# Optimization experiments

Measured on AMD Instinct MI355X. Metric: run time of the kernel, lower is better.

The kernel has to match this reference:

```python
import jax, jax.numpy as jnp
import numpy as np
import math

MU = 5; ETA = 1.0; ITERS = 3
SIGMA_C = 1.0; SIGMA_S = 1.6 * SIGMA_C
SIGMA_M = 3.0; RHO = 0.99; TAU = 0.7
MAX_T = int(math.floor(3 * SIGMA_C))  # 3
MAX_S = int(math.floor(3 * SIGMA_M))  # 9
DELTA = 1.0
B, C, X, Y = 4, 1, 512, 512


def _gpdf(v, sig):
    return math.exp(-v * v / (2.0 * sig * sig)) / (math.sqrt(2.0 * math.pi) * sig)


def _sobel(img):
    k = jnp.array([[-1., -2., -1.], [0., 0., 0.], [1., 2., 1.]], dtype=img.dtype)
    kern = jnp.stack([k, k.T])[:, None]  # [2,1,3,3] OIHW
    return jax.lax.conv_general_dilated(img, kern, (1, 1), [(1, 1), (1, 1)],
                                        dimension_numbers=('NCHW', 'OIHW', 'NCHW'))


def _gather_flat(arr, idx):
    # arr [b,c,x,y], idx int [b,x,y] flattened spatial index (px*Y+py)
    b, c, x, y = arr.shape
    flat = arr.reshape(b, c, x * y)
    idxb = jnp.broadcast_to(idx.reshape(b, 1, x * y), (b, c, x * y))
    return jnp.take_along_axis(flat, idxb, axis=2).reshape(b, c, x, y)


def _safe_norm(v):
    m = jnp.linalg.norm(v, axis=1, keepdims=True)
    return v / jnp.where(m == 0, 1.0, m)


def _etf(images):
    b, c, x, y = images.shape
    sob = _sobel(images)                                   # [b,2,x,y]
    mag = jnp.linalg.norm(sob, axis=1, keepdims=True)      # [b,1,x,y]
    mag = mag / jnp.max(mag)
    mag_p = jnp.pad(mag, ((0, 0), (0, 0), (MU, MU), (MU, MU)))
    sobel_X = mag[:, None]                                 # [b,1,1,x,y]
    tang = _safe_norm(jnp.stack([-sob[:, 1], sob[:, 0]], axis=1))
    K = 2 * MU + 1
    for _ in range(ITERS):
        for ori in ('V', 'H'):
            tang_p = jnp.pad(tang, ((0, 0), (0, 0), (MU, MU), (MU, MU)))
            tang_X = tang[:, None]                         # [b,1,2,x,y]
            if ori == 'V':
                tang_Y = jnp.stack([tang_p[:, :, i:i + x, MU:MU + y] for i in range(K)], axis=1)
                sobel_Y = jnp.stack([mag_p[:, :, i:i + x, MU:MU + y] for i in range(K)], axis=1)
            else:
                tang_Y = jnp.stack([tang_p[:, :, MU:MU + x, i:i + y] for i in range(K)], axis=1)
                sobel_Y = jnp.stack([mag_p[:, :, MU:MU + x, i:i + y] for i in range(K)], axis=1)
            # weight: magnitude term * direction term / 2
            w = (jnp.tanh(ETA * (sobel_Y - sobel_X)) + 1.0) \
                * jnp.sum(tang_X * tang_Y, axis=2, keepdims=True) * 0.5
            tang = _safe_norm(jnp.sum(tang_Y * w, axis=1))
    return tang


def _dog(images, etf):
    b, c, x, y = images.shape
    xi, yi = jnp.meshgrid(jnp.arange(x, dtype=images.dtype),
                          jnp.arange(y, dtype=images.dtype), indexing='ij')
    idx0 = jnp.broadcast_to(jnp.stack([xi, yi])[None], (b, 2, x, y))
    per = jnp.stack([-etf[:, 1], etf[:, 0]], axis=1)       # perpendicular to flow
    dog = jnp.zeros_like(images)
    tw = 0.0
    for t in range(-MAX_T, MAX_T + 1):
        pts = idx0 + DELTA * per * t
        px = jnp.round(jnp.clip(pts[:, 0], 0, x - 1)).astype(jnp.int32)
        py = jnp.round(jnp.clip(pts[:, 1], 0, y - 1)).astype(jnp.int32)
        il = _gather_flat(images, px * y + py)
        gw = _gpdf(t, SIGMA_C) - RHO * _gpdf(t, SIGMA_S)
        tw += gw
        dog = dog + il * gw
    return dog / tw


def _fdog_float(images):
    b, c, x, y = images.shape
    etf = _etf(images)
    dog = _dog(images, etf)
    fdog = jnp.zeros_like(images)
    tw = 0.0
    xi, yi = jnp.meshgrid(jnp.arange(x, dtype=jnp.int32),
                          jnp.arange(y, dtype=jnp.int32), indexing='ij')
    for s_dir in (-1, 1):
        px = jnp.broadcast_to(xi[None], (b, x, y))
        py = jnp.broadcast_to(yi[None], (b, x, y))
        for s in range(0 if s_dir == 1 else 1, MAX_S + 1):
            if s != 0:
                p_etf = _gather_flat(etf, px * y + py)     # flow at current points
                fx = px.astype(images.dtype) + DELTA * p_etf[:, 0] * s_dir
                fy = py.astype(images.dtype) + DELTA * p_etf[:, 1] * s_dir
                px = jnp.round(jnp.clip(fx, 0, x - 1)).astype(jnp.int32)
                py = jnp.round(jnp.clip(fy, 0, y - 1)).astype(jnp.int32)
            f_s = _gather_flat(dog, px * y + py)
            gw = _gpdf(s, SIGMA_M)
            tw += gw
            fdog = fdog + f_s * gw
    return fdog / tw


def setup_inputs() -> dict:
    key = jax.random.key(0)
    images = jax.random.uniform(key, (B, C, X, Y), dtype=jnp.float32)
    return {"images": images}


def reference(images):
    fdog = _fdog_float(images)
    edges = ~((fdog < 0) & (1.0 + jnp.tanh(fdog) < TAU))
    return edges.astype(jnp.int32)
```

## Files before the change

kernel.cpp:

```cpp
#include <hip/hip_runtime.h>
#include <math.h>

#pragma clang fp contract(off)

#define BN 4
#define SX 512
#define SY 512
#define NPIX (BN * SX * SY)
#define MU 5
#define MB (1024 * 1024)
#define NBLOCKS 2048

struct DogW  { float g[7];  float tw; };
struct FdogW { float g[10]; float tw; };

__device__ __forceinline__ float fast_tanh_f32(float dF) {
    double d = (double)dF;
    double y = fabs(d);
    double t = expm1(2.0 * y);
    double r = t / (t + 2.0);
    if (y > 350.0) r = 1.0;
    return (float)copysign(r, d);
}

__device__ __forceinline__ float img_at(const float* __restrict__ img, int b, int x, int y) {
    if (x < 0 || x >= SX || y < 0 || y >= SY) return 0.0f;
    return img[(size_t)b * SX * SY + (size_t)x * SY + y];
}

#define SLAB_DECODE                                   \
    int slab = blockIdx.x;                            \
    int b    = slab >> 1;                             \
    int xi   = ((slab & 1) << 8) + blockIdx.y;        \
    size_t base = (size_t)b * SX * SY;                \
    size_t rowb = base + (size_t)xi * SY;

__global__ __launch_bounds__(256) void k_sobel(const float* __restrict__ img,
                                               float* __restrict__ mag,
                                               float2* __restrict__ tang,
                                               float* __restrict__ partial) {
#pragma clang fp contract(off)
    SLAB_DECODE
    float bmax = 0.0f;
#pragma unroll
    for (int half = 0; half < 2; ++half) {
        int yi = (int)threadIdx.x + half * 256;

        float v00 = img_at(img, b, xi - 1, yi - 1);
        float v01 = img_at(img, b, xi - 1, yi    );
        float v02 = img_at(img, b, xi - 1, yi + 1);
        float v10 = img_at(img, b, xi,     yi - 1);
        float v12 = img_at(img, b, xi,     yi + 1);
        float v20 = img_at(img, b, xi + 1, yi - 1);
        float v21 = img_at(img, b, xi + 1, yi    );
        float v22 = img_at(img, b, xi + 1, yi + 1);

        float s0 = (-1.0f * v00);
        s0 = s0 + (-2.0f * v01);
        s0 = s0 + (-1.0f * v02);
        s0 = s0 + ( 1.0f * v20);
        s0 = s0 + ( 2.0f * v21);
        s0 = s0 + ( 1.0f * v22);
        float s1 = (-1.0f * v00);
        s1 = s1 + ( 1.0f * v02);
        s1 = s1 + (-2.0f * v10);
        s1 = s1 + ( 2.0f * v12);
        s1 = s1 + (-1.0f * v20);
        s1 = s1 + ( 1.0f * v22);

        float m = sqrtf((s0 * s0) + (s1 * s1));
        mag[rowb + yi] = m;

        float tx = -s1, ty = s0;
        float n = sqrtf((tx * tx) + (ty * ty));
        float d = (n == 0.0f) ? 1.0f : n;
        tang[rowb + yi] = make_float2(tx / d, ty / d);
        bmax = fmaxf(bmax, m);
    }

    for (int off = 32; off > 0; off >>= 1) bmax = fmaxf(bmax, __shfl_down(bmax, off, 64));
    __shared__ float red[4];
    int lane = threadIdx.x & 63;
    int wid  = threadIdx.x >> 6;
    if (lane == 0) red[wid] = bmax;
    __syncthreads();
    if (threadIdx.x == 0) {
        float bm = fmaxf(fmaxf(red[0], red[1]), fmaxf(red[2], red[3]));
        partial[blockIdx.x + 8 * blockIdx.y] = bm;
    }
}

__global__ void k_reduce(const float* __restrict__ partial, unsigned int* __restrict__ maxbits) {
    float m = 0.0f;
    for (int i = threadIdx.x; i < NBLOCKS; i += 256) m = fmaxf(m, partial[i]);
    for (int off = 32; off > 0; off >>= 1) m = fmaxf(m, __shfl_down(m, off, 64));
    __shared__ float red[4];
    int lane = threadIdx.x & 63;
    int wid  = threadIdx.x >> 6;
    if (lane == 0) red[wid] = m;
    __syncthreads();
    if (threadIdx.x == 0) {
        float bm = fmaxf(fmaxf(red[0], red[1]), fmaxf(red[2], red[3]));
        *maxbits = __float_as_uint(bm);
    }
}

__global__ void k_norm(float* __restrict__ mag, const unsigned int* __restrict__ maxbits) {
    int i = blockIdx.x * blockDim.x + threadIdx.x;
    float mx = __uint_as_float(*maxbits);
    mag[i] = mag[i] / mx;
}

__global__ __launch_bounds__(256) void k_tanh(const float* __restrict__ mag,
                                              const unsigned int* __restrict__ maxbits,
                                              float* __restrict__ TV, float* __restrict__ TH) {
#pragma clang fp contract(off)
    SLAB_DECODE
    float mx = __uint_as_float(*maxbits);
#pragma unroll
    for (int half = 0; half < 2; ++half) {
        int yi = (int)threadIdx.x + half * 256;
        size_t idx = rowb + yi;
        float cm = mag[idx] / mx;
#pragma unroll
        for (int k = 1; k <= 5; ++k) {
            if (xi + k < SX) {
                float nm = mag[idx + (size_t)k * SY] / mx;
                TV[(size_t)(k - 1) * NPIX + idx] = fast_tanh_f32(nm - cm);
            }
        }
#pragma unroll
        for (int k = 1; k <= 5; ++k) {
            if (yi + k < SY) {
                float nm = mag[idx + k] / mx;
                TH[(size_t)(k - 1) * NPIX + idx] = fast_tanh_f32(nm - cm);
            }
        }
    }
}

__global__ __launch_bounds__(256) void k_etf_v(const float2* __restrict__ tsrc,
                                               float2* __restrict__ tdst,
                                               const float* __restrict__ TV) {
#pragma clang fp contract(off)
    SLAB_DECODE
#pragma unroll
    for (int half = 0; half < 2; ++half) {
        int yi = (int)threadIdx.x + half * 256;
        size_t idx = rowb + yi;
        float2 ct = tsrc[idx];

        float sx = 0.0f, sy = 0.0f;
#pragma unroll
        for (int k = -MU; k <= MU; ++k) {
            int nx = xi + k;
            if (nx < 0 || nx >= SX) continue;
            size_t nidx = idx + (size_t)k * SY;
            float2 nt = tsrc[nidx];
            float th;
            if (k > 0)      th =  TV[(size_t)(k - 1) * NPIX + idx];
            else if (k < 0) th = -TV[(size_t)(-k - 1) * NPIX + nidx];
            else            th =  0.0f;
            float dot = (ct.x * nt.x) + (ct.y * nt.y);
            float w   = ((th + 1.0f) * dot) * 0.5f;
            sx = sx + (nt.x * w);
            sy = sy + (nt.y * w);
        }
        float n = sqrtf((sx * sx) + (sy * sy));
        float d = (n == 0.0f) ? 1.0f : n;
        tdst[idx] = make_float2(sx / d, sy / d);
    }
}

__global__ __launch_bounds__(256) void k_etf_h(const float2* __restrict__ tsrc,
                                               float2* __restrict__ tdst,
                                               const float* __restrict__ TH) {
#pragma clang fp contract(off)
    SLAB_DECODE
    int tid = threadIdx.x;

    __shared__ __align__(16) float2 sT[SY];
    __shared__ __align__(16) float  sTH[5][SY];

    ((float4*)sT)[tid] = ((const float4*)(tsrc + rowb))[tid];
    for (int i = tid; i < 5 * (SY / 4); i += 256) {
        int j = i >> 7;
        int c = i & 127;
        ((float4*)&sTH[0][0])[i] = ((const float4*)(TH + (size_t)j * NPIX + rowb))[c];
    }
    __syncthreads();

#pragma unroll
    for (int half = 0; half < 2; ++half) {
        int yi = tid + half * 256;
        float2 ct = sT[yi];
        float sx = 0.0f, sy = 0.0f;
#pragma unroll
        for (int k = -MU; k <= MU; ++k) {
            int ny = yi + k;
            if (ny < 0 || ny >= SY) continue;
            float2 nt = sT[ny];
            float th;
            if (k > 0)      th =  sTH[k - 1][yi];
            else if (k < 0) th = -sTH[-k - 1][ny];
            else            th =  0.0f;
            float dot = (ct.x * nt.x) + (ct.y * nt.y);
            float w   = ((th + 1.0f) * dot) * 0.5f;
            sx = sx + (nt.x * w);
            sy = sy + (nt.y * w);
        }
        float n = sqrtf((sx * sx) + (sy * sy));
        float d = (n == 0.0f) ? 1.0f : n;
        tdst[rowb + yi] = make_float2(sx / d, sy / d);
    }
}

__global__ void k_etf(const float2* __restrict__ tsrc, float2* __restrict__ tdst,
                      const float* __restrict__ mag, int vert) {
#pragma clang fp contract(off)
    int yi = blockIdx.x * blockDim.x + threadIdx.x;
    int xi = blockIdx.y;
    int b  = blockIdx.z;
    size_t base = (size_t)b * SX * SY;
    size_t idx  = base + (size_t)xi * SY + yi;

    float  cm = mag[idx];
    float2 ct = tsrc[idx];

    float sx = 0.0f, sy = 0.0f;
    for (int k = -MU; k <= MU; ++k) {
        int nx = xi + (vert ? k : 0);
        int ny = yi + (vert ? 0 : k);
        if (nx < 0 || nx >= SX || ny < 0 || ny >= SY) continue;
        size_t nidx = base + (size_t)nx * SY + ny;
        float  nm = mag[nidx];
        float2 nt = tsrc[nidx];
        float dot = (ct.x * nt.x) + (ct.y * nt.y);
        float th  = (float)tanh((double)(nm - cm));
        float w   = ((th + 1.0f) * dot) * 0.5f;
        sx = sx + (nt.x * w);
        sy = sy + (nt.y * w);
    }
    float n = sqrtf((sx * sx) + (sy * sy));
    float d = (n == 0.0f) ? 1.0f : n;
    tdst[idx] = make_float2(sx / d, sy / d);
}

__global__ __launch_bounds__(256) void k_dog(const float* __restrict__ img,
                                             const float2* __restrict__ etf,
                                             float* __restrict__ dog, DogW w) {
#pragma clang fp contract(off)
    SLAB_DECODE
#pragma unroll
    for (int half = 0; half < 2; ++half) {
        int yi = (int)threadIdx.x + half * 256;
        size_t idx = rowb + yi;

        float2 e = etf[idx];
        float perx = -e.y;
        float pery =  e.x;
        float xf = (float)xi, yf = (float)yi;

        float acc = 0.0f;
#pragma unroll
        for (int t = -3; t <= 3; ++t) {
            float tf  = (float)t;
            float ptx = xf + (perx * tf);
            float pty = yf + (pery * tf);
            int px = (int)rintf(fminf(fmaxf(ptx, 0.0f), (float)(SX - 1)));
            int py = (int)rintf(fminf(fmaxf(pty, 0.0f), (float)(SY - 1)));
            float il = img[base + (size_t)px * SY + py];
            acc = acc + (il * w.g[t + 3]);
        }
        dog[idx] = acc / w.tw;
    }
}

__global__ __launch_bounds__(256) void k_fdog(const float* __restrict__ dog,
                                              const float2* __restrict__ etf,
                                              int* __restrict__ out, FdogW w) {
#pragma clang fp contract(off)
    SLAB_DECODE
    for (int half = 0; half < 2; ++half) {
        int yi = (int)threadIdx.x + half * 256;
        size_t idx = rowb + yi;

        float d1[9];
        float d2[10];
        float2 e0 = etf[idx];
        float2 e1 = e0, e2 = e0;
        int p1x = xi, p1y = yi;
        int p2x = xi, p2y = yi;
        d2[0] = dog[idx];

#pragma unroll
        for (int s = 1; s <= 9; ++s) {
            float fx1 = (float)p1x + (e1.x * -1.0f);
            float fy1 = (float)p1y + (e1.y * -1.0f);
            p1x = (int)rintf(fminf(fmaxf(fx1, 0.0f), (float)(SX - 1)));
            p1y = (int)rintf(fminf(fmaxf(fy1, 0.0f), (float)(SY - 1)));
            size_t i1 = base + (size_t)p1x * SY + p1y;
            float fx2 = (float)p2x + (e2.x * 1.0f);
            float fy2 = (float)p2y + (e2.y * 1.0f);
            p2x = (int)rintf(fminf(fmaxf(fx2, 0.0f), (float)(SX - 1)));
            p2y = (int)rintf(fminf(fmaxf(fy2, 0.0f), (float)(SY - 1)));
            size_t i2 = base + (size_t)p2x * SY + p2y;

            d1[s - 1] = dog[i1];
            d2[s]     = dog[i2];
            if (s < 9) {
                e1 = etf[i1];
                e2 = etf[i2];
            }
        }

        float acc = 0.0f;
#pragma unroll
        for (int s = 1; s <= 9; ++s) acc = acc + (d1[s - 1] * w.g[s]);
        acc = acc + (d2[0] * w.g[0]);
#pragma unroll
        for (int s = 1; s <= 9; ++s) acc = acc + (d2[s] * w.g[s]);

        float fv = acc / w.tw;
        float th = 1.0f + fast_tanh_f32(fv);
        out[idx] = ((fv < 0.0f) && (th < 0.7f)) ? 0 : 1;
    }
}

static double gpdf(double v, double sig) {
    return exp(-(v * v) / (2.0 * sig * sig)) / (sqrt(2.0 * M_PI) * sig);
}

extern "C" void kernel_launch(void* const* d_in, const int* in_sizes, int n_in,
                              void* d_out, int out_size, void* d_ws, size_t ws_size,
                              hipStream_t stream) {
    const float* img = (const float*)d_in[0];
    int* out = (int*)d_out;
    char* ws = (char*)d_ws;

    const size_t need = (size_t)60 * MB + NBLOCKS * sizeof(float) + 4;
    bool fast = ws_size >= need;

    float*  mag = (float*)(ws);
    float2* tA  = (float2*)(ws + (size_t)4  * MB);
    float2* tB  = (float2*)(ws + (size_t)12 * MB);
    float*  dog = (float*)(ws + (size_t)12 * MB);
    float*  TV  = (float*)(ws + (size_t)20 * MB);
    float*  TH  = (float*)(ws + (size_t)40 * MB);
    size_t  tail = fast ? (size_t)60 * MB : (size_t)20 * MB;
    float*        partial = (float*)(ws + tail);
    unsigned int* maxbits = (unsigned int*)(ws + tail + NBLOCKS * sizeof(float));

    dim3 blk(256, 1, 1);
    dim3 sgrd(8, 256, 1);

    k_sobel<<<sgrd, blk, 0, stream>>>(img, mag, tA, partial);
    k_reduce<<<1, 256, 0, stream>>>(partial, maxbits);

    float2* src = tA;
    float2* dst = tB;
    if (fast) {
        k_tanh<<<sgrd, blk, 0, stream>>>(mag, maxbits, TV, TH);
        for (int it = 0; it < 3; ++it) {
            k_etf_v<<<sgrd, blk, 0, stream>>>(src, dst, TV);
            { float2* t = src; src = dst; dst = t; }
            k_etf_h<<<sgrd, blk, 0, stream>>>(src, dst, TH);
            { float2* t = src; src = dst; dst = t; }
        }
    } else {
        dim3 grd(SY / 256, SX, BN);
        k_norm<<<NPIX / 256, 256, 0, stream>>>(mag, maxbits);
        for (int it = 0; it < 3; ++it) {
            k_etf<<<grd, blk, 0, stream>>>(src, dst, mag, 1);
            { float2* t = src; src = dst; dst = t; }
            k_etf<<<grd, blk, 0, stream>>>(src, dst, mag, 0);
            { float2* t = src; src = dst; dst = t; }
        }
    }
    float* dogbuf = (src == tA) ? dog : (float*)tA;

    DogW dw;
    {
        double tw = 0.0;
        for (int t = -3; t <= 3; ++t) {
            double g = gpdf((double)t, 1.0) - 0.99 * gpdf((double)t, 1.6);
            dw.g[t + 3] = (float)g;
            tw += g;
        }
        dw.tw = (float)tw;
    }
    k_dog<<<sgrd, blk, 0, stream>>>(img, src, dogbuf, dw);

    FdogW fw;
    {
        for (int s = 0; s <= 9; ++s) fw.g[s] = (float)gpdf((double)s, 3.0);
        double tw = 0.0;
        for (int s = 1; s <= 9; ++s) tw += gpdf((double)s, 3.0);
        for (int s = 0; s <= 9; ++s) tw += gpdf((double)s, 3.0);
        fw.tw = (float)tw;
    }
    k_fdog<<<sgrd, blk, 0, stream>>>(dogbuf, src, out, fw);
}
```

Measured before the change: 205.5 us.

## Fuse whole pipeline into one cooperative persistent kernel with grid syncs

```diff
diff --git a/kernel.cpp b/kernel.cpp
--- a/kernel.cpp
+++ b/kernel.cpp
@@ -1,5 +1,8 @@
 #include <hip/hip_runtime.h>
+#include <hip/hip_cooperative_groups.h>
 #include <math.h>
+
+namespace cg = cooperative_groups;
 
 #pragma clang fp contract(off)
 
@@ -9,6 +12,7 @@
 #define NPIX (BN * SX * SY)
 #define MU 5
 #define MB (1024 * 1024)
+#define GRID_BLKS 512
 #define NBLOCKS 2048
 
 struct DogW  { float g[7];  float tw; };
@@ -28,23 +32,29 @@
     return img[(size_t)b * SX * SY + (size_t)x * SY + y];
 }
 
-#define SLAB_DECODE                                   \
-    int slab = blockIdx.x;                            \
-    int b    = slab >> 1;                             \
-    int xi   = ((slab & 1) << 8) + blockIdx.y;        \
-    size_t base = (size_t)b * SX * SY;                \
-    size_t rowb = base + (size_t)xi * SY;
-
-__global__ __launch_bounds__(256) void k_sobel(const float* __restrict__ img,
-                                               float* __restrict__ mag,
-                                               float2* __restrict__ tang,
-                                               float* __restrict__ partial) {
-#pragma clang fp contract(off)
-    SLAB_DECODE
+__global__ __launch_bounds__(256, 2) void k_fused(
+    const float* __restrict__ img, float* __restrict__ mag,
+    float2* __restrict__ tA, float2* __restrict__ tB,
+    float* __restrict__ TV, float* __restrict__ TH,
+    float* __restrict__ partial, float* __restrict__ dogbuf,
+    int* __restrict__ out, DogW dw, FdogW fw)
+{
+#pragma clang fp contract(off)
+    cg::grid_group grid = cg::this_grid();
+    const int tid = (int)threadIdx.x;
+    const int nthreads = (int)gridDim.x * 256;
+    const int gid0 = (int)blockIdx.x * 256 + tid;
+
+    __shared__ float red[4];
+    __shared__ float smax;
+    const int lane = tid & 63;
+    const int wid  = tid >> 6;
+
     float bmax = 0.0f;
-#pragma unroll
-    for (int half = 0; half < 2; ++half) {
-        int yi = (int)threadIdx.x + half * 256;
+    for (int id = gid0; id < NPIX; id += nthreads) {
+        int yi = id & (SY - 1);
+        int xi = (id >> 9) & (SX - 1);
+        int b  = id >> 18;
 
         float v00 = img_at(img, b, xi - 1, yi - 1);
         float v01 = img_at(img, b, xi - 1, yi    );
@@ -69,15 +79,224 @@
         s1 = s1 + ( 1.0f * v22);
 
         float m = sqrtf((s0 * s0) + (s1 * s1));
+        mag[id] = m;
+
+        float tx = -s1, ty = s0;
+        float n = sqrtf((tx * tx) + (ty * ty));
+        float d = (n == 0.0f) ? 1.0f : n;
+        tA[id] = make_float2(tx / d, ty / d);
+        bmax = fmaxf(bmax, m);
+    }
+    for (int off = 32; off > 0; off >>= 1) bmax = fmaxf(bmax, __shfl_down(bmax, off, 64));
+    if (lane == 0) red[wid] = bmax;
+    __syncthreads();
+    if (tid == 0) partial[blockIdx.x] = fmaxf(fmaxf(red[0], red[1]), fmaxf(red[2], red[3]));
+    grid.sync();
+
+    {
+        float m = 0.0f;
+        for (int i = tid; i < (int)gridDim.x; i += 256) m = fmaxf(m, partial[i]);
+        for (int off = 32; off > 0; off >>= 1) m = fmaxf(m, __shfl_down(m, off, 64));
+        if (lane == 0) red[wid] = m;
+        __syncthreads();
+        if (tid == 0) smax = fmaxf(fmaxf(red[0], red[1]), fmaxf(red[2], red[3]));
+        __syncthreads();
+    }
+    const float mx = smax;
+
+    for (int id = gid0; id < NPIX; id += nthreads) {
+        int yi = id & (SY - 1);
+        int xi = (id >> 9) & (SX - 1);
+        float cm = mag[id] / mx;
+#pragma unroll
+        for (int k = 1; k <= 5; ++k) {
+            if (xi + k < SX) {
+                float nm = mag[id + k * SY] / mx;
+                TV[(size_t)(k - 1) * NPIX + id] = fast_tanh_f32(nm - cm);
+            }
+        }
+#pragma unroll
+        for (int k = 1; k <= 5; ++k) {
+            if (yi + k < SY) {
+                float nm = mag[id + k] / mx;
+                TH[(size_t)(k - 1) * NPIX + id] = fast_tanh_f32(nm - cm);
+            }
+        }
+    }
+    grid.sync();
+
+    float2* src = tA;
+    float2* dst = tB;
+    for (int it = 0; it < 3; ++it) {
+        for (int id = gid0; id < NPIX; id += nthreads) {
+            int xi = (id >> 9) & (SX - 1);
+            float2 ct = src[id];
+            float sx = 0.0f, sy = 0.0f;
+#pragma unroll
+            for (int k = -MU; k <= MU; ++k) {
+                int nx = xi + k;
+                if (nx < 0 || nx >= SX) continue;
+                int nidx = id + k * SY;
+                float2 nt = src[nidx];
+                float th;
+                if (k > 0)      th =  TV[(size_t)(k - 1) * NPIX + id];
+                else if (k < 0) th = -TV[(size_t)(-k - 1) * NPIX + nidx];
+                else            th =  0.0f;
+                float dot = (ct.x * nt.x) + (ct.y * nt.y);
+                float w   = ((th + 1.0f) * dot) * 0.5f;
+                sx = sx + (nt.x * w);
+                sy = sy + (nt.y * w);
+            }
+            float n = sqrtf((sx * sx) + (sy * sy));
+            float d = (n == 0.0f) ? 1.0f : n;
+            dst[id] = make_float2(sx / d, sy / d);
+        }
+        grid.sync();
+        { float2* t = src; src = dst; dst = t; }
+
+        bool last = (it == 2);
+        for (int id = gid0; id < NPIX; id += nthreads) {
+            int yi = id & (SY - 1);
+            float2 ct = src[id];
+            float sx = 0.0f, sy = 0.0f;
+#pragma unroll
+            for (int k = -MU; k <= MU; ++k) {
+                int ny = yi + k;
+                if (ny < 0 || ny >= SY) continue;
+                int nidx = id + k;
+                float2 nt = src[nidx];
+                float th;
+                if (k > 0)      th =  TH[(size_t)(k - 1) * NPIX + id];
+                else if (k < 0) th = -TH[(size_t)(-k - 1) * NPIX + nidx];
+                else            th =  0.0f;
+                float dot = (ct.x * nt.x) + (ct.y * nt.y);
+                float w   = ((th + 1.0f) * dot) * 0.5f;
+                sx = sx + (nt.x * w);
+                sy = sy + (nt.y * w);
+            }
+            float n = sqrtf((sx * sx) + (sy * sy));
+            float d = (n == 0.0f) ? 1.0f : n;
+            float ex = sx / d, ey = sy / d;
+            dst[id] = make_float2(ex, ey);
+
+            if (last) {
+                int xi = (id >> 9) & (SX - 1);
+                int b  = id >> 18;
+                size_t base = (size_t)b << 18;
+                float perx = -ey, pery = ex;
+                float xf = (float)xi, yf = (float)yi;
+                float acc = 0.0f;
+#pragma unroll
+                for (int t = -3; t <= 3; ++t) {
+                    float tf  = (float)t;
+                    float ptx = xf + (perx * tf);
+                    float pty = yf + (pery * tf);
+                    int px = (int)rintf(fminf(fmaxf(ptx, 0.0f), (float)(SX - 1)));
+                    int py = (int)rintf(fminf(fmaxf(pty, 0.0f), (float)(SY - 1)));
+                    float il = img[base + (size_t)px * SY + py];
+                    acc = acc + (il * dw.g[t + 3]);
+                }
+                dogbuf[id] = acc / dw.tw;
+            }
+        }
+        grid.sync();
+        { float2* t = src; src = dst; dst = t; }
+    }
+
+    const float2* etf = src;
+    for (int id = gid0; id < NPIX; id += nthreads) {
+        int yi = id & (SY - 1);
+        int xi = (id >> 9) & (SX - 1);
+        int b  = id >> 18;
+        size_t base = (size_t)b << 18;
+
+        float d1[9];
+        float d2[10];
+        float2 e0 = etf[id];
+        float2 e1 = e0, e2 = e0;
+        int p1x = xi, p1y = yi;
+        int p2x = xi, p2y = yi;
+        d2[0] = dogbuf[id];
+
+#pragma unroll
+        for (int s = 1; s <= 9; ++s) {
+            float fx1 = (float)p1x + (e1.x * -1.0f);
+            float fy1 = (float)p1y + (e1.y * -1.0f);
+            p1x = (int)rintf(fminf(fmaxf(fx1, 0.0f), (float)(SX - 1)));
+            p1y = (int)rintf(fminf(fmaxf(fy1, 0.0f), (float)(SY - 1)));
+            size_t i1 = base + (size_t)p1x * SY + p1y;
+            float fx2 = (float)p2x + (e2.x * 1.0f);
+            float fy2 = (float)p2y + (e2.y * 1.0f);
+            p2x = (int)rintf(fminf(fmaxf(fx2, 0.0f), (float)(SX - 1)));
+            p2y = (int)rintf(fminf(fmaxf(fy2, 0.0f), (float)(SY - 1)));
+            size_t i2 = base + (size_t)p2x * SY + p2y;
+
+            d1[s - 1] = dogbuf[i1];
+            d2[s]     = dogbuf[i2];
+            if (s < 9) {
+                e1 = etf[i1];
+                e2 = etf[i2];
+            }
+        }
+
+        float acc = 0.0f;
+#pragma unroll
+        for (int s = 1; s <= 9; ++s) acc = acc + (d1[s - 1] * fw.g[s]);
+        acc = acc + (d2[0] * fw.g[0]);
+#pragma unroll
+        for (int s = 1; s <= 9; ++s) acc = acc + (d2[s] * fw.g[s]);
+
+        float fv = acc / fw.tw;
+        float th = 1.0f + fast_tanh_f32(fv);
+        out[id] = ((fv < 0.0f) && (th < 0.7f)) ? 0 : 1;
+    }
+}
+
+#define SLAB_DECODE                                   \
+    int slab = blockIdx.x;                            \
+    int b    = slab >> 1;                             \
+    int xi   = ((slab & 1) << 8) + blockIdx.y;        \
+    size_t base = (size_t)b * SX * SY;                \
+    size_t rowb = base + (size_t)xi * SY;
+
+__global__ __launch_bounds__(256) void k_sobel(const float* __restrict__ img,
+                                               float* __restrict__ mag,
+                                               float2* __restrict__ tang,
+                                               float* __restrict__ partial) {
+#pragma clang fp contract(off)
+    SLAB_DECODE
+    float bmax = 0.0f;
+#pragma unroll
+    for (int half = 0; half < 2; ++half) {
+        int yi = (int)threadIdx.x + half * 256;
+        float v00 = img_at(img, b, xi - 1, yi - 1);
+        float v01 = img_at(img, b, xi - 1, yi    );
+        float v02 = img_at(img, b, xi - 1, yi + 1);
+        float v10 = img_at(img, b, xi,     yi - 1);
+        float v12 = img_at(img, b, xi,     yi + 1);
+        float v20 = img_at(img, b, xi + 1, yi - 1);
+        float v21 = img_at(img, b, xi + 1, yi    );
+        float v22 = img_at(img, b, xi + 1, yi + 1);
+        float s0 = (-1.0f * v00);
+        s0 = s0 + (-2.0f * v01);
+        s0 = s0 + (-1.0f * v02);
+        s0 = s0 + ( 1.0f * v20);
+        s0 = s0 + ( 2.0f * v21);
+        s0 = s0 + ( 1.0f * v22);
+        float s1 = (-1.0f * v00);
+        s1 = s1 + ( 1.0f * v02);
+        s1 = s1 + (-2.0f * v10);
+        s1 = s1 + ( 2.0f * v12);
+        s1 = s1 + (-1.0f * v20);
+        s1 = s1 + ( 1.0f * v22);
+        float m = sqrtf((s0 * s0) + (s1 * s1));
         mag[rowb + yi] = m;
-
         float tx = -s1, ty = s0;
         float n = sqrtf((tx * tx) + (ty * ty));
         float d = (n == 0.0f) ? 1.0f : n;
         tang[rowb + yi] = make_float2(tx / d, ty / d);
         bmax = fmaxf(bmax, m);
     }
-
     for (int off = 32; off > 0; off >>= 1) bmax = fmaxf(bmax, __shfl_down(bmax, off, 64));
     __shared__ float red[4];
     int lane = threadIdx.x & 63;
@@ -85,8 +304,8 @@
     if (lane == 0) red[wid] = bmax;
     __syncthreads();
     if (threadIdx.x == 0) {
-        float bm = fmaxf(fmaxf(red[0], red[1]), fmaxf(red[2], red[3]));
-        partial[blockIdx.x + 8 * blockIdx.y] = bm;
+        partial[blockIdx.x + 8 * blockIdx.y] =
+            fmaxf(fmaxf(red[0], red[1]), fmaxf(red[2], red[3]));
     }
 }
 
@@ -99,16 +318,8 @@
     int wid  = threadIdx.x >> 6;
     if (lane == 0) red[wid] = m;
     __syncthreads();
-    if (threadIdx.x == 0) {
-        float bm = fmaxf(fmaxf(red[0], red[1]), fmaxf(red[2], red[3]));
-        *maxbits = __float_as_uint(bm);
-    }
-}
-
-__global__ void k_norm(float* __restrict__ mag, const unsigned int* __restrict__ maxbits) {
-    int i = blockIdx.x * blockDim.x + threadIdx.x;
-    float mx = __uint_as_float(*maxbits);
-    mag[i] = mag[i] / mx;
+    if (threadIdx.x == 0)
+        *maxbits = __float_as_uint(fmaxf(fmaxf(red[0], red[1]), fmaxf(red[2], red[3])));
 }
 
 __global__ __launch_bounds__(256) void k_tanh(const float* __restrict__ mag,
@@ -149,7 +360,6 @@
         int yi = (int)threadIdx.x + half * 256;
         size_t idx = rowb + yi;
         float2 ct = tsrc[idx];
-
         float sx = 0.0f, sy = 0.0f;
 #pragma unroll
         for (int k = -MU; k <= MU; ++k) {
@@ -215,37 +425,6 @@
     }
 }
 
-__global__ void k_etf(const float2* __restrict__ tsrc, float2* __restrict__ tdst,
-                      const float* __restrict__ mag, int vert) {
-#pragma clang fp contract(off)
-    int yi = blockIdx.x * blockDim.x + threadIdx.x;
-    int xi = blockIdx.y;
-    int b  = blockIdx.z;
-    size_t base = (size_t)b * SX * SY;
-    size_t idx  = base + (size_t)xi * SY + yi;
-
-    float  cm = mag[idx];
-    float2 ct = tsrc[idx];
-
-    float sx = 0.0f, sy = 0.0f;
-    for (int k = -MU; k <= MU; ++k) {
-        int nx = xi + (vert ? k : 0);
-        int ny = yi + (vert ? 0 : k);
-        if (nx < 0 || nx >= SX || ny < 0 || ny >= SY) continue;
-        size_t nidx = base + (size_t)nx * SY + ny;
-        float  nm = mag[nidx];
-        float2 nt = tsrc[nidx];
-        float dot = (ct.x * nt.x) + (ct.y * nt.y);
-        float th  = (float)tanh((double)(nm - cm));
-        float w   = ((th + 1.0f) * dot) * 0.5f;
-        sx = sx + (nt.x * w);
-        sy = sy + (nt.y * w);
-    }
-    float n = sqrtf((sx * sx) + (sy * sy));
-    float d = (n == 0.0f) ? 1.0f : n;
-    tdst[idx] = make_float2(sx / d, sy / d);
-}
-
 __global__ __launch_bounds__(256) void k_dog(const float* __restrict__ img,
                                              const float2* __restrict__ etf,
                                              float* __restrict__ dog, DogW w) {
@@ -255,12 +434,10 @@
     for (int half = 0; half < 2; ++half) {
         int yi = (int)threadIdx.x + half * 256;
         size_t idx = rowb + yi;
-
         float2 e = etf[idx];
         float perx = -e.y;
         float pery =  e.x;
         float xf = (float)xi, yf = (float)yi;
-
         float acc = 0.0f;
 #pragma unroll
         for (int t = -3; t <= 3; ++t) {
@@ -284,7 +461,6 @@
     for (int half = 0; half < 2; ++half) {
         int yi = (int)threadIdx.x + half * 256;
         size_t idx = rowb + yi;
-
         float d1[9];
         float d2[10];
         float2 e0 = etf[idx];
@@ -292,7 +468,6 @@
         int p1x = xi, p1y = yi;
         int p2x = xi, p2y = yi;
         d2[0] = dog[idx];
-
 #pragma unroll
         for (int s = 1; s <= 9; ++s) {
             float fx1 = (float)p1x + (e1.x * -1.0f);
@@ -305,7 +480,6 @@
             p2x = (int)rintf(fminf(fmaxf(fx2, 0.0f), (float)(SX - 1)));
             p2y = (int)rintf(fminf(fmaxf(fy2, 0.0f), (float)(SY - 1)));
             size_t i2 = base + (size_t)p2x * SY + p2y;
-
             d1[s - 1] = dog[i1];
             d2[s]     = dog[i2];
             if (s < 9) {
@@ -313,14 +487,12 @@
                 e2 = etf[i2];
             }
         }
-
         float acc = 0.0f;
 #pragma unroll
         for (int s = 1; s <= 9; ++s) acc = acc + (d1[s - 1] * w.g[s]);
         acc = acc + (d2[0] * w.g[0]);
 #pragma unroll
         for (int s = 1; s <= 9; ++s) acc = acc + (d2[s] * w.g[s]);
-
         float fv = acc / w.tw;
         float th = 1.0f + fast_tanh_f32(fv);
         out[idx] = ((fv < 0.0f) && (th < 0.7f)) ? 0 : 1;
@@ -338,46 +510,17 @@
     int* out = (int*)d_out;
     char* ws = (char*)d_ws;
 
-    const size_t need = (size_t)60 * MB + NBLOCKS * sizeof(float) + 4;
-    bool fast = ws_size >= need;
+    const size_t need = (size_t)64 * MB + NBLOCKS * sizeof(float) + 4;
+    (void)need;
 
     float*  mag = (float*)(ws);
     float2* tA  = (float2*)(ws + (size_t)4  * MB);
     float2* tB  = (float2*)(ws + (size_t)12 * MB);
-    float*  dog = (float*)(ws + (size_t)12 * MB);
     float*  TV  = (float*)(ws + (size_t)20 * MB);
     float*  TH  = (float*)(ws + (size_t)40 * MB);
-    size_t  tail = fast ? (size_t)60 * MB : (size_t)20 * MB;
-    float*        partial = (float*)(ws + tail);
-    unsigned int* maxbits = (unsigned int*)(ws + tail + NBLOCKS * sizeof(float));
-
-    dim3 blk(256, 1, 1);
-    dim3 sgrd(8, 256, 1);
-
-    k_sobel<<<sgrd, blk, 0, stream>>>(img, mag, tA, partial);
-    k_reduce<<<1, 256, 0, stream>>>(partial, maxbits);
-
-    float2* src = tA;
-    float2* dst = tB;
-    if (fast) {
-        k_tanh<<<sgrd, blk, 0, stream>>>(mag, maxbits, TV, TH);
-        for (int it = 0; it < 3; ++it) {
-            k_etf_v<<<sgrd, blk, 0, stream>>>(src, dst, TV);
-            { float2* t = src; src = dst; dst = t; }
-            k_etf_h<<<sgrd, blk, 0, stream>>>(src, dst, TH);
-            { float2* t = src; src = dst; dst = t; }
-        }
-    } else {
-        dim3 grd(SY / 256, SX, BN);
-        k_norm<<<NPIX / 256, 256, 0, stream>>>(mag, maxbits);
-        for (int it = 0; it < 3; ++it) {
-            k_etf<<<grd, blk, 0, stream>>>(src, dst, mag, 1);
-            { float2* t = src; src = dst; dst = t; }
-            k_etf<<<grd, blk, 0, stream>>>(src, dst, mag, 0);
-            { float2* t = src; src = dst; dst = t; }
-        }
-    }
-    float* dogbuf = (src == tA) ? dog : (float*)tA;
+    float*  dog = (float*)(ws + (size_t)60 * MB);
+    float*        partial = (float*)(ws + (size_t)64 * MB);
+    unsigned int* maxbits = (unsigned int*)(ws + (size_t)64 * MB + NBLOCKS * sizeof(float));
 
     DogW dw;
     {
@@ -389,8 +532,6 @@
         }
         dw.tw = (float)tw;
     }
-    k_dog<<<sgrd, blk, 0, stream>>>(img, src, dogbuf, dw);
-
     FdogW fw;
     {
         for (int s = 0; s <= 9; ++s) fw.g[s] = (float)gpdf((double)s, 3.0);
@@ -399,5 +540,33 @@
         for (int s = 0; s <= 9; ++s) tw += gpdf((double)s, 3.0);
         fw.tw = (float)tw;
     }
-    k_fdog<<<sgrd, blk, 0, stream>>>(dogbuf, src, out, fw);
-}
+
+    {
+        void* args[] = { (void*)&img, (void*)&mag, (void*)&tA, (void*)&tB,
+                         (void*)&TV, (void*)&TH, (void*)&partial, (void*)&dog,
+                         (void*)&out, (void*)&dw, (void*)&fw };
+        hipError_t err = hipLaunchCooperativeKernel((const void*)k_fused,
+                                                    dim3(GRID_BLKS), dim3(256),
+                                                    args, 0, stream);
+        if (err == hipSuccess) return;
+        (void)hipGetLastError();
+    }
+
+    dim3 blk(256, 1, 1);
+    dim3 sgrd(8, 256, 1);
+
+    k_sobel<<<sgrd, blk, 0, stream>>>(img, mag, tA, partial);
+    k_reduce<<<1, 256, 0, stream>>>(partial, maxbits);
+    k_tanh<<<sgrd, blk, 0, stream>>>(mag, maxbits, TV, TH);
+
+    float2* src = tA;
+    float2* dst = tB;
+    for (int it = 0; it < 3; ++it) {
+        k_etf_v<<<sgrd, blk, 0, stream>>>(src, dst, TV);
+        { float2* t = src; src = dst; dst = t; }
+        k_etf_h<<<sgrd, blk, 0, stream>>>(src, dst, TH);
+        { float2* t = src; src = dst; dst = t; }
+    }
+    k_dog<<<sgrd, blk, 0, stream>>>(img, src, dog, dw);
+    k_fdog<<<sgrd, blk, 0, stream>>>(dog, src, out, fw);
+}
```

After: 761.4 us. 270% more time.
